# Performance work log

Measured on AMD Instinct MI355X. Metric: run time of the kernel, lower is better.

The kernel has to match this reference:

```python
import jax, jax.numpy as jnp
import numpy as np

WS = 8        # window size
NUM_HEADS = 4 # attention heads


def setup_inputs() -> dict:
    key = jax.random.key(0)
    k1, k2, k3 = jax.random.split(key, 3)
    B, N, C = 32, 4096, 128
    x = jax.random.normal(k1, (B, N, C), dtype=jnp.float32)
    w_qkv = jax.random.normal(k2, (3 * C, C), dtype=jnp.float32) * (C ** -0.5)
    w_proj = jax.random.normal(k3, (C, C), dtype=jnp.float32) * (C ** -0.5)
    b_proj = jnp.zeros((C,), dtype=jnp.float32)
    return {"x": x, "w_qkv": w_qkv, "w_proj": w_proj, "b_proj": b_proj, "H": 64, "W": 64}


def reference(x, w_qkv, w_proj, b_proj, H, W):
    B, N, C = x.shape
    ws, nh = WS, NUM_HEADS
    hd = C // nh
    scale = hd ** -0.5
    hg, wg = H // ws, W // ws
    G = hg * wg          # total windows
    S = ws * ws          # tokens per window
    # partition into windows: [B, hg, ws, wg, ws, C] -> [B, G, S, C]
    xg = x.reshape(B, hg, ws, wg, ws, C).transpose(0, 1, 3, 2, 4, 5).reshape(B, G, S, C)
    # qkv projection (no bias)
    qkv = jnp.einsum('bgsc,oc->bgso', xg, w_qkv)
    qkv = qkv.reshape(B, G, S, 3, nh, hd).transpose(3, 0, 1, 4, 2, 5)  # [3,B,G,nh,S,hd]
    q, k, v = qkv[0], qkv[1], qkv[2]
    attn = jnp.einsum('bgnsd,bgntd->bgnst', q, k) * scale
    attn = jax.nn.softmax(attn, axis=-1)
    out = jnp.einsum('bgnst,bgntd->bgnsd', attn, v)
    # [B,G,nh,S,hd] -> [B,G,S,C] -> un-window -> [B,N,C]
    out = out.transpose(0, 1, 3, 2, 4).reshape(B, hg, wg, ws, ws, C)
    out = out.transpose(0, 1, 3, 2, 4, 5).reshape(B, N, C)
    return jnp.einsum('bnc,oc->bno', out, w_proj) + b_proj
```

## Files before the change

kernel.cpp:

```cpp
#include <hip/hip_runtime.h>
#include <hip/hip_bf16.h>
#include <cstdint>

typedef short short8 __attribute__((ext_vector_type(8)));
typedef float floatx4 __attribute__((ext_vector_type(4)));
typedef unsigned short ushortx4 __attribute__((ext_vector_type(4)));
typedef unsigned int uintx4 __attribute__((ext_vector_type(4)));

#define MFMA16B(A, B, C) __builtin_amdgcn_mfma_f32_16x16x32_bf16((A), (B), (C), 0, 0, 0)
#define LDS_FENCE() asm volatile("" ::: "memory")

__device__ __forceinline__ unsigned short f2bf(float f) {
  union { float f; unsigned u; } v; v.f = f;
  unsigned r = v.u + 0x7FFFu + ((v.u >> 16) & 1u);
  return (unsigned short)(r >> 16);
}
__device__ __forceinline__ unsigned pack_bf2(float a, float b) {
  __hip_bfloat162 h = __float22bfloat162_rn(float2{a, b});
  union { __hip_bfloat162 h; unsigned u; } c; c.h = h; return c.u;
}
__device__ __forceinline__ float lo_half_f(unsigned u) {
  union { unsigned u; float f; } c; c.u = u << 16; return c.f;
}
__device__ __forceinline__ float hi_half_f(unsigned u) {
  union { unsigned u; float f; } c; c.u = u & 0xffff0000u; return c.f;
}
__device__ __forceinline__ ushortx4 pack_bf4(float a, float b, float c, float d) {
  uint2 p; p.x = pack_bf2(a, b); p.y = pack_bf2(c, d);
  union { uint2 u; ushortx4 s; } v; v.u = p; return v.s;
}

__global__ void __launch_bounds__(256) prep_weights(const float* __restrict__ wq,
                                                    const float* __restrict__ wp,
                                                    unsigned short* __restrict__ wq_h,
                                                    unsigned short* __restrict__ wp_h) {
  int i = blockIdx.x * 256 + threadIdx.x;
  if (i < 384 * 128) wq_h[i] = f2bf(wq[i]);
  if (i < 128 * 128) wp_h[i] = f2bf(wp[i]);
}

__global__ void __launch_bounds__(256, 3) win_attn(const float* __restrict__ x,
                                                   const unsigned short* __restrict__ wqh,
                                                   const unsigned short* __restrict__ wph,
                                                   const float* __restrict__ bias,
                                                   float* __restrict__ out) {
  __shared__ char smem[49152];
  const int tid = threadIdx.x;
  const int wv = tid >> 6, lane = tid & 63, lr = lane & 15, lg = lane >> 4;
  const int bid = blockIdx.x;
  const int b = bid >> 6, g = bid & 63, gh = g >> 3, gw = g & 7;
  const size_t base = (size_t)b * (4096 * 128);

  {
    const int r = tid >> 2, c0 = (tid & 3) * 32;
    const int n = gh * 512 + (r >> 3) * 64 + gw * 8 + (r & 7);
    const float4* xp = (const float4*)(x + base + (size_t)n * 128 + c0);
    const int rb = r * 512, sz = (r & 7) << 4;
#pragma unroll
    for (int i = 0; i < 4; ++i) {
      float4 u = xp[2 * i], w = xp[2 * i + 1];
      unsigned h0 = pack_bf2(u.x, u.y), h1 = pack_bf2(u.z, u.w);
      unsigned h2 = pack_bf2(w.x, w.y), h3 = pack_bf2(w.z, w.w);
      unsigned l0 = pack_bf2(u.x - lo_half_f(h0), u.y - hi_half_f(h0));
      unsigned l1 = pack_bf2(u.z - lo_half_f(h1), u.w - hi_half_f(h1));
      unsigned l2 = pack_bf2(w.x - lo_half_f(h2), w.y - hi_half_f(h2));
      unsigned l3 = pack_bf2(w.z - lo_half_f(h3), w.w - hi_half_f(h3));
      uintx4 hv = {h0, h1, h2, h3}, lv = {l0, l1, l2, l3};
      *(uintx4*)(smem + ((rb + (c0 + 8 * i) * 2) ^ sz)) = hv;
      *(uintx4*)(smem + ((rb + 256 + (c0 + 8 * i) * 2) ^ sz)) = lv;
    }
  }
  __syncthreads();

  const int swzx = (lr & 7) << 4;
  const float SCALE = 0.17677669529663687f;

  ushortx4 pk[6][4];
#pragma unroll
  for (int j = 0; j < 6; ++j) {
    const int m = j >> 1, jt = j & 1;
    const unsigned short* wb = wqh + (size_t)(m * 128 + wv * 32 + jt * 16 + lr) * 128 + lg * 8;
    short8 bw[4];
    bw[0] = *(const short8*)(wb);
    bw[1] = *(const short8*)(wb + 32);
    bw[2] = *(const short8*)(wb + 64);
    bw[3] = *(const short8*)(wb + 96);
    const float fs = (j < 2) ? SCALE : 1.0f;
#pragma unroll
    for (int mt = 0; mt < 4; ++mt) {
      const int rbase = (16 * mt + lr) * 512 + lg * 16;
      floatx4 acc = {0.f, 0.f, 0.f, 0.f};
#pragma unroll
      for (int kk = 0; kk < 8; ++kk) {
        short8 a = *(const short8*)(smem + ((rbase + kk * 64) ^ swzx));
        acc = MFMA16B(a, bw[kk & 3], acc);
      }
      pk[j][mt] = pack_bf4(acc[0] * fs, acc[1] * fs, acc[2] * fs, acc[3] * fs);
    }
  }
  __syncthreads();

  char* const wbase = smem + wv * 12288;
#pragma unroll
  for (int j = 0; j < 4; ++j) {
    char* qk = wbase + (j >> 1) * 4096;
    const int d = (j & 1) * 16 + lr;
#pragma unroll
    for (int mt = 0; mt < 4; ++mt)
#pragma unroll
      for (int r = 0; r < 4; ++r) {
        const int s = 16 * mt + 4 * lg + r;
        *(unsigned short*)(qk + ((s * 64 + d * 2) ^ ((s & 3) << 4))) = pk[j][mt][r];
      }
  }
#pragma unroll
  for (int jt = 0; jt < 2; ++jt) {
    const int d = jt * 16 + lr;
#pragma unroll
    for (int mt = 0; mt < 4; ++mt)
      *(ushortx4*)(wbase + 8192 + ((d * 128 + (16 * mt + 4 * lg) * 2) ^ ((d & 7) << 4))) =
          pk[4 + jt][mt];
  }
  LDS_FENCE();

  const int swzq = (lr & 3) << 4, swzp = (lr & 7) << 4;
  short8 ka[4], qb[4];
#pragma unroll
  for (int i = 0; i < 4; ++i) {
    const int ro = (16 * i + lr) * 64 + lg * 16;
    qb[i] = *(const short8*)(wbase + (ro ^ swzq));
    ka[i] = *(const short8*)(wbase + 4096 + (ro ^ swzq));
  }
  floatx4 sc[4][4];
#pragma unroll
  for (int mt = 0; mt < 4; ++mt)
#pragma unroll
    for (int nt = 0; nt < 4; ++nt) {
      floatx4 z = {0.f, 0.f, 0.f, 0.f};
      sc[mt][nt] = MFMA16B(ka[mt], qb[nt], z);
    }

  float inv[4];
#pragma unroll
  for (int nt = 0; nt < 4; ++nt) {
    float m0 = -1e30f;
#pragma unroll
    for (int mt = 0; mt < 4; ++mt)
#pragma unroll
      for (int r = 0; r < 4; ++r) m0 = fmaxf(m0, sc[mt][nt][r]);
    m0 = fmaxf(m0, __shfl_xor(m0, 16));
    m0 = fmaxf(m0, __shfl_xor(m0, 32));
    float s0 = 0.f;
#pragma unroll
    for (int mt = 0; mt < 4; ++mt)
#pragma unroll
      for (int r = 0; r < 4; ++r) {
        float e = __expf(sc[mt][nt][r] - m0);
        sc[mt][nt][r] = e;
        s0 += e;
      }
    s0 += __shfl_xor(s0, 16);
    s0 += __shfl_xor(s0, 32);
    inv[nt] = 1.f / s0;
  }

#pragma unroll
  for (int nt = 0; nt < 4; ++nt) {
    const int rb = (16 * nt + lr) * 128;
#pragma unroll
    for (int mt = 0; mt < 4; ++mt)
      *(ushortx4*)(wbase + ((rb + (16 * mt + 4 * lg) * 2) ^ swzp)) =
          pack_bf4(sc[mt][nt][0] * inv[nt], sc[mt][nt][1] * inv[nt],
                   sc[mt][nt][2] * inv[nt], sc[mt][nt][3] * inv[nt]);
  }
  LDS_FENCE();

  short8 va[2][2], pb[4][2];
#pragma unroll
  for (int dt = 0; dt < 2; ++dt)
#pragma unroll
    for (int ks = 0; ks < 2; ++ks)
      va[dt][ks] = *(const short8*)(wbase + 8192 +
                   (((16 * dt + lr) * 128 + ks * 64 + lg * 16) ^ swzp));
#pragma unroll
  for (int st = 0; st < 4; ++st)
#pragma unroll
    for (int ks = 0; ks < 2; ++ks)
      pb[st][ks] = *(const short8*)(wbase +
                   (((16 * st + lr) * 128 + ks * 64 + lg * 16) ^ swzp));
  floatx4 ot[2][4];
#pragma unroll
  for (int dt = 0; dt < 2; ++dt)
#pragma unroll
    for (int st = 0; st < 4; ++st) {
      floatx4 z = {0.f, 0.f, 0.f, 0.f};
      z = MFMA16B(va[dt][0], pb[st][0], z);
      ot[dt][st] = MFMA16B(va[dt][1], pb[st][1], z);
    }

  __syncthreads();

#pragma unroll
  for (int st = 0; st < 4; ++st)
#pragma unroll
    for (int dt = 0; dt < 2; ++dt)
      *(ushortx4*)(smem + (16 * st + lr) * 272 + (wv * 32 + dt * 16 + 4 * lg) * 2) =
          pack_bf4(ot[dt][st][0], ot[dt][st][1], ot[dt][st][2], ot[dt][st][3]);
  __syncthreads();

  short8 ao[4];
#pragma unroll
  for (int kk = 0; kk < 4; ++kk)
    ao[kk] = *(const short8*)(smem + (16 * wv + lr) * 272 + kk * 64 + lg * 16);
#pragma unroll
  for (int nt = 0; nt < 8; ++nt) {
    const unsigned short* wb = wph + (size_t)(nt * 16 + lr) * 128 + lg * 8;
    floatx4 acc = {0.f, 0.f, 0.f, 0.f};
    acc = MFMA16B(ao[0], *(const short8*)(wb), acc);
    acc = MFMA16B(ao[1], *(const short8*)(wb + 32), acc);
    acc = MFMA16B(ao[2], *(const short8*)(wb + 64), acc);
    acc = MFMA16B(ao[3], *(const short8*)(wb + 96), acc);
    const float bb = bias[nt * 16 + lr];
#pragma unroll
    for (int r = 0; r < 4; ++r) {
      const int s0 = 16 * wv + 4 * lg + r;
      const int n = gh * 512 + (s0 >> 3) * 64 + gw * 8 + (s0 & 7);
      out[base + (size_t)n * 128 + nt * 16 + lr] = acc[r] + bb;
    }
  }
}

extern "C" void kernel_launch(void* const* d_in, const int* in_sizes, int n_in,
                              void* d_out, int out_size, void* d_ws, size_t ws_size,
                              hipStream_t stream) {
  (void)in_sizes; (void)n_in; (void)out_size; (void)ws_size;
  const float* x  = (const float*)d_in[0];
  const float* wq = (const float*)d_in[1];
  const float* wp = (const float*)d_in[2];
  const float* bp = (const float*)d_in[3];
  float* out = (float*)d_out;
  unsigned short* wq_h = (unsigned short*)d_ws;
  unsigned short* wp_h = wq_h + 384 * 128;
  prep_weights<<<192, 256, 0, stream>>>(wq, wp, wq_h, wp_h);
  win_attn<<<2048, 256, 0, stream>>>(x, wq_h, wp_h, bp, out);
}
```

Baseline: 223.4 us.

## Cut register pressure: stream V to LDS, split accumulators, per-column softmax

V projection results are now written straight to a separate LDS region instead of being held in registers until after a barrier. The hi/lo split-bf16 accumulation uses two independent MFMA chains that are summed at the end, which shortens the dependent chain. Softmax is computed one query column at a time, and each column is written to LDS immediately, so the full 4x4 score tile is never live at once. The LDS layout changes (qk and v regions separate, 8-way swizzle on Q/K). The aim is lower VGPR usage and better MFMA overlap, at the cost of more LDS traffic interleaved with compute.

New measurement: 346.5 us. 1.55x slower.

```diff
diff --git a/kernel.cpp b/kernel.cpp
--- a/kernel.cpp
+++ b/kernel.cpp
@@ -75,79 +75,81 @@
   const int swzx = (lr & 7) << 4;
   const float SCALE = 0.17677669529663687f;
 
-  ushortx4 pk[6][4];
+  char* const qkbase = smem + wv * 8192;
+  char* const vbase  = smem + 32768 + wv * 4096;
+
+  ushortx4 pk[4][4];
 #pragma unroll
   for (int j = 0; j < 6; ++j) {
-    const int m = j >> 1, jt = j & 1;
-    const unsigned short* wb = wqh + (size_t)(m * 128 + wv * 32 + jt * 16 + lr) * 128 + lg * 8;
-    short8 bw[4];
-    bw[0] = *(const short8*)(wb);
-    bw[1] = *(const short8*)(wb + 32);
-    bw[2] = *(const short8*)(wb + 64);
-    bw[3] = *(const short8*)(wb + 96);
+    const int jt = j & 1;
+    const unsigned short* wb =
+        wqh + (size_t)((j >> 1) * 128 + wv * 32 + jt * 16 + lr) * 128 + lg * 8;
+    short8 bw0 = *(const short8*)(wb);
+    short8 bw1 = *(const short8*)(wb + 32);
+    short8 bw2 = *(const short8*)(wb + 64);
+    short8 bw3 = *(const short8*)(wb + 96);
     const float fs = (j < 2) ? SCALE : 1.0f;
 #pragma unroll
     for (int mt = 0; mt < 4; ++mt) {
       const int rbase = (16 * mt + lr) * 512 + lg * 16;
-      floatx4 acc = {0.f, 0.f, 0.f, 0.f};
-#pragma unroll
-      for (int kk = 0; kk < 8; ++kk) {
-        short8 a = *(const short8*)(smem + ((rbase + kk * 64) ^ swzx));
-        acc = MFMA16B(a, bw[kk & 3], acc);
+      floatx4 aH = {0.f, 0.f, 0.f, 0.f}, aL = {0.f, 0.f, 0.f, 0.f};
+      aH = MFMA16B(*(const short8*)(smem + ((rbase) ^ swzx)), bw0, aH);
+      aH = MFMA16B(*(const short8*)(smem + ((rbase + 64) ^ swzx)), bw1, aH);
+      aH = MFMA16B(*(const short8*)(smem + ((rbase + 128) ^ swzx)), bw2, aH);
+      aH = MFMA16B(*(const short8*)(smem + ((rbase + 192) ^ swzx)), bw3, aH);
+      aL = MFMA16B(*(const short8*)(smem + ((rbase + 256) ^ swzx)), bw0, aL);
+      aL = MFMA16B(*(const short8*)(smem + ((rbase + 320) ^ swzx)), bw1, aL);
+      aL = MFMA16B(*(const short8*)(smem + ((rbase + 384) ^ swzx)), bw2, aL);
+      aL = MFMA16B(*(const short8*)(smem + ((rbase + 448) ^ swzx)), bw3, aL);
+      floatx4 acc = aH + aL;
+      if (j < 4) {
+        pk[j][mt] = pack_bf4(acc[0] * fs, acc[1] * fs, acc[2] * fs, acc[3] * fs);
+      } else {
+        const int d = jt * 16 + lr;
+        *(ushortx4*)(vbase + ((d * 128 + (16 * mt + 4 * lg) * 2) ^ ((d & 7) << 4))) =
+            pack_bf4(acc[0], acc[1], acc[2], acc[3]);
       }
-      pk[j][mt] = pack_bf4(acc[0] * fs, acc[1] * fs, acc[2] * fs, acc[3] * fs);
-    }
-  }
-  __syncthreads();
-
-  char* const wbase = smem + wv * 12288;
+    }
+  }
+  __syncthreads();
+
 #pragma unroll
   for (int j = 0; j < 4; ++j) {
-    char* qk = wbase + (j >> 1) * 4096;
+    char* qk = qkbase + (j >> 1) * 4096;
     const int d = (j & 1) * 16 + lr;
 #pragma unroll
     for (int mt = 0; mt < 4; ++mt)
 #pragma unroll
       for (int r = 0; r < 4; ++r) {
         const int s = 16 * mt + 4 * lg + r;
-        *(unsigned short*)(qk + ((s * 64 + d * 2) ^ ((s & 3) << 4))) = pk[j][mt][r];
+        *(unsigned short*)(qk + ((s * 64 + d * 2) ^ ((s & 7) << 4))) = pk[j][mt][r];
       }
   }
-#pragma unroll
-  for (int jt = 0; jt < 2; ++jt) {
-    const int d = jt * 16 + lr;
-#pragma unroll
-    for (int mt = 0; mt < 4; ++mt)
-      *(ushortx4*)(wbase + 8192 + ((d * 128 + (16 * mt + 4 * lg) * 2) ^ ((d & 7) << 4))) =
-          pk[4 + jt][mt];
-  }
   LDS_FENCE();
 
-  const int swzq = (lr & 3) << 4, swzp = (lr & 7) << 4;
-  short8 ka[4], qb[4];
-#pragma unroll
-  for (int i = 0; i < 4; ++i) {
-    const int ro = (16 * i + lr) * 64 + lg * 16;
-    qb[i] = *(const short8*)(wbase + (ro ^ swzq));
-    ka[i] = *(const short8*)(wbase + 4096 + (ro ^ swzq));
-  }
-  floatx4 sc[4][4];
-#pragma unroll
-  for (int mt = 0; mt < 4; ++mt)
-#pragma unroll
-    for (int nt = 0; nt < 4; ++nt) {
+  const int swzp = (lr & 7) << 4;
+  short8 ka[4];
+#pragma unroll
+  for (int i = 0; i < 4; ++i)
+    ka[i] = *(const short8*)(qkbase + 4096 + (((16 * i + lr) * 64 + lg * 16) ^ swzp));
+  short8 qb0 = *(const short8*)(qkbase + (((lr) * 64 + lg * 16) ^ swzp));
+  short8 qb1 = *(const short8*)(qkbase + (((16 + lr) * 64 + lg * 16) ^ swzp));
+  short8 qb2 = *(const short8*)(qkbase + (((32 + lr) * 64 + lg * 16) ^ swzp));
+  short8 qb3 = *(const short8*)(qkbase + (((48 + lr) * 64 + lg * 16) ^ swzp));
+  LDS_FENCE();
+
+  auto softcol = [&](int nt, short8 qbv) {
+    floatx4 sc4[4];
+#pragma unroll
+    for (int mt = 0; mt < 4; ++mt) {
       floatx4 z = {0.f, 0.f, 0.f, 0.f};
-      sc[mt][nt] = MFMA16B(ka[mt], qb[nt], z);
-    }
-
-  float inv[4];
-#pragma unroll
-  for (int nt = 0; nt < 4; ++nt) {
+      sc4[mt] = MFMA16B(ka[mt], qbv, z);
+    }
     float m0 = -1e30f;
 #pragma unroll
     for (int mt = 0; mt < 4; ++mt)
 #pragma unroll
-      for (int r = 0; r < 4; ++r) m0 = fmaxf(m0, sc[mt][nt][r]);
+      for (int r = 0; r < 4; ++r) m0 = fmaxf(m0, sc4[mt][r]);
     m0 = fmaxf(m0, __shfl_xor(m0, 16));
     m0 = fmaxf(m0, __shfl_xor(m0, 32));
     float s0 = 0.f;
@@ -155,48 +157,43 @@
     for (int mt = 0; mt < 4; ++mt)
 #pragma unroll
       for (int r = 0; r < 4; ++r) {
-        float e = __expf(sc[mt][nt][r] - m0);
-        sc[mt][nt][r] = e;
+        float e = __expf(sc4[mt][r] - m0);
+        sc4[mt][r] = e;
         s0 += e;
       }
     s0 += __shfl_xor(s0, 16);
     s0 += __shfl_xor(s0, 32);
-    inv[nt] = 1.f / s0;
-  }
-
-#pragma unroll
-  for (int nt = 0; nt < 4; ++nt) {
+    const float inv = 1.f / s0;
     const int rb = (16 * nt + lr) * 128;
 #pragma unroll
     for (int mt = 0; mt < 4; ++mt)
-      *(ushortx4*)(wbase + ((rb + (16 * mt + 4 * lg) * 2) ^ swzp)) =
-          pack_bf4(sc[mt][nt][0] * inv[nt], sc[mt][nt][1] * inv[nt],
-                   sc[mt][nt][2] * inv[nt], sc[mt][nt][3] * inv[nt]);
-  }
-  LDS_FENCE();
-
-  short8 va[2][2], pb[4][2];
-#pragma unroll
-  for (int dt = 0; dt < 2; ++dt)
-#pragma unroll
-    for (int ks = 0; ks < 2; ++ks)
-      va[dt][ks] = *(const short8*)(wbase + 8192 +
-                   (((16 * dt + lr) * 128 + ks * 64 + lg * 16) ^ swzp));
-#pragma unroll
-  for (int st = 0; st < 4; ++st)
-#pragma unroll
-    for (int ks = 0; ks < 2; ++ks)
-      pb[st][ks] = *(const short8*)(wbase +
-                   (((16 * st + lr) * 128 + ks * 64 + lg * 16) ^ swzp));
+      *(ushortx4*)(qkbase + ((rb + (16 * mt + 4 * lg) * 2) ^ swzp)) =
+          pack_bf4(sc4[mt][0] * inv, sc4[mt][1] * inv, sc4[mt][2] * inv,
+                   sc4[mt][3] * inv);
+    LDS_FENCE();
+  };
+  softcol(0, qb0);
+  softcol(1, qb1);
+  softcol(2, qb2);
+  softcol(3, qb3);
+
+  short8 va00 = *(const short8*)(vbase + (((lr) * 128 + lg * 16) ^ swzp));
+  short8 va01 = *(const short8*)(vbase + (((lr) * 128 + 64 + lg * 16) ^ swzp));
+  short8 va10 = *(const short8*)(vbase + (((16 + lr) * 128 + lg * 16) ^ swzp));
+  short8 va11 = *(const short8*)(vbase + (((16 + lr) * 128 + 64 + lg * 16) ^ swzp));
   floatx4 ot[2][4];
 #pragma unroll
-  for (int dt = 0; dt < 2; ++dt)
-#pragma unroll
-    for (int st = 0; st < 4; ++st) {
-      floatx4 z = {0.f, 0.f, 0.f, 0.f};
-      z = MFMA16B(va[dt][0], pb[st][0], z);
-      ot[dt][st] = MFMA16B(va[dt][1], pb[st][1], z);
-    }
+  for (int st = 0; st < 4; ++st) {
+    const int pr = (16 * st + lr) * 128;
+    short8 pb0 = *(const short8*)(qkbase + ((pr + lg * 16) ^ swzp));
+    short8 pb1 = *(const short8*)(qkbase + ((pr + 64 + lg * 16) ^ swzp));
+    floatx4 z0 = {0.f, 0.f, 0.f, 0.f};
+    floatx4 t0 = MFMA16B(va00, pb0, z0);
+    ot[0][st] = MFMA16B(va01, pb1, t0);
+    floatx4 z1 = {0.f, 0.f, 0.f, 0.f};
+    floatx4 t1 = MFMA16B(va10, pb0, z1);
+    ot[1][st] = MFMA16B(va11, pb1, t1);
+  }
 
   __syncthreads();
 
@@ -208,18 +205,18 @@
           pack_bf4(ot[dt][st][0], ot[dt][st][1], ot[dt][st][2], ot[dt][st][3]);
   __syncthreads();
 
-  short8 ao[4];
-#pragma unroll
-  for (int kk = 0; kk < 4; ++kk)
-    ao[kk] = *(const short8*)(smem + (16 * wv + lr) * 272 + kk * 64 + lg * 16);
+  short8 ao0 = *(const short8*)(smem + (16 * wv + lr) * 272 + lg * 16);
+  short8 ao1 = *(const short8*)(smem + (16 * wv + lr) * 272 + 64 + lg * 16);
+  short8 ao2 = *(const short8*)(smem + (16 * wv + lr) * 272 + 128 + lg * 16);
+  short8 ao3 = *(const short8*)(smem + (16 * wv + lr) * 272 + 192 + lg * 16);
 #pragma unroll
   for (int nt = 0; nt < 8; ++nt) {
     const unsigned short* wb = wph + (size_t)(nt * 16 + lr) * 128 + lg * 8;
     floatx4 acc = {0.f, 0.f, 0.f, 0.f};
-    acc = MFMA16B(ao[0], *(const short8*)(wb), acc);
-    acc = MFMA16B(ao[1], *(const short8*)(wb + 32), acc);
-    acc = MFMA16B(ao[2], *(const short8*)(wb + 64), acc);
-    acc = MFMA16B(ao[3], *(const short8*)(wb + 96), acc);
+    acc = MFMA16B(ao0, *(const short8*)(wb), acc);
+    acc = MFMA16B(ao1, *(const short8*)(wb + 32), acc);
+    acc = MFMA16B(ao2, *(const short8*)(wb + 64), acc);
+    acc = MFMA16B(ao3, *(const short8*)(wb + 96), acc);
     const float bb = bias[nt * 16 + lr];
 #pragma unroll
     for (int r = 0; r < 4; ++r) {
```
